# Kernel optimization log

Hardware: AMD Instinct MI355X
Metric: run time of the kernel (lower is better)

## Reference

```python
import jax, jax.numpy as jnp
import numpy as np

G = 1024        # graphs in batch
NPG = 64        # nodes per graph
EPG = 256       # edges per graph
N = G * NPG     # 65536 total nodes
E = G * EPG     # 262144 total edges
IN_CH = 768
CH = 128
RATIO = 0.5
K = int(RATIO * EPG)  # edges reserved as 'causal' per graph


def setup_inputs() -> dict:
    key = jax.random.key(0)
    ks = jax.random.split(key, 10)
    w = lambda k, shape, fan: (jax.random.normal(k, shape, jnp.float32) / np.float32(np.sqrt(fan)))
    x = jax.random.normal(ks[0], (N, IN_CH), jnp.float32)
    # per-graph random edges, offset into the global node index space
    ei = jax.random.randint(ks[1], (2, G, EPG), 0, NPG)
    edge_index = (ei + (jnp.arange(G) * NPG)[None, :, None]).reshape(2, -1).astype(jnp.int32)
    edge_attr = jax.random.uniform(ks[2], (E,), jnp.float32)  # positive edge weights
    batch = jnp.repeat(jnp.arange(G, dtype=jnp.int32), NPG)
    return dict(
        x=x, edge_index=edge_index, edge_attr=edge_attr, batch=batch,
        W1=w(ks[3], (IN_CH, CH), IN_CH), V1=w(ks[4], (IN_CH, CH), IN_CH), b1=jnp.zeros((CH,), jnp.float32),
        W2=w(ks[5], (CH, CH), CH),       V2=w(ks[6], (CH, CH), CH),       b2=jnp.zeros((CH,), jnp.float32),
        mw1=w(ks[7], (2 * CH, 4 * CH), 2 * CH), mb1=jnp.zeros((4 * CH,), jnp.float32),
        mw2=w(ks[8], (4 * CH, 1), 4 * CH),      mb2=jnp.zeros((1,), jnp.float32),
    )


def reference(x, edge_index, edge_attr, batch, W1, V1, b1, W2, V2, b2, mw1, mb1, mw2, mb2):
    row, col = edge_index[0], edge_index[1]
    ew = edge_attr.reshape(-1)

    # gcn_norm (symmetric, no self loops), as used inside ARMAConv
    deg = jnp.zeros((N,), x.dtype).at[col].add(ew)
    dis = jnp.where(deg > 0, jax.lax.rsqrt(jnp.where(deg > 0, deg, 1.0)), 0.0)
    norm = dis[row] * ew * dis[col]  # [E]

    def arma(h, W, V, b):
        # ARMAConv, num_stacks=1, num_layers=1: ReLU(A_hat (h W) + h V + b)
        m = h @ W                                            # [N, C]
        agg = jnp.zeros((N, W.shape[1]), h.dtype).at[col].add(norm[:, None] * m[row])
        return jax.nn.relu(agg + h @ V + b)

    x1 = jax.nn.relu(arma(x, W1, V1, b1))  # outer F.relu (idempotent after internal ReLU)
    x2 = arma(x1, W2, V2, b2)              # [N, CH]

    # edge-gather MLP -> scalar score per edge
    edge_rep = jnp.concatenate([x2[row], x2[col]], axis=-1)          # [E, 2C]
    pred_edge_weight = (jax.nn.relu(edge_rep @ mw1 + mb1) @ mw2 + mb2).reshape(-1)  # [E]

    # per-graph top-k split (batched replacement of the numpy argpartition loop)
    wg = pred_edge_weight.reshape(G, EPG)
    order = jnp.argsort(-wg, axis=1)                                  # descending
    base = (jnp.arange(G) * EPG)[:, None]
    cid = (base + order[:, :K]).reshape(-1)   # causal (reserved) edge ids
    did = (base + order[:, K:]).reshape(-1)   # conf (dropped) edge ids

    causal = (x2, edge_index[:, cid], edge_attr[cid], pred_edge_weight[cid], batch)
    conf = (x2, edge_index[:, did], edge_attr[did], -pred_edge_weight[did], batch)
    return (*causal, *conf, pred_edge_weight)
```

## Files before the change

### kernel.cpp

```cpp
#include <hip/hip_runtime.h>
#include <hip/hip_bf16.h>
#include <stdint.h>

#define G_    1024
#define NPG   64
#define EPG   256
#define N_    (G_*NPG)
#define E_    (G_*EPG)
#define IN_CH 768
#define CH    128
#define KSEL  128
#define HID   512

#define NCH  (N_*CH)
#define GK   (G_*KSEL)
#define OFF0 0
#define OFF1 (OFF0 + NCH)
#define OFF2 (OFF1 + 2*GK)
#define OFF3 (OFF2 + GK)
#define OFF4 (OFF3 + GK)
#define OFF5 (OFF4 + N_)
#define OFF6 (OFF5 + NCH)
#define OFF7 (OFF6 + 2*GK)
#define OFF8 (OFF7 + GK)
#define OFF9 (OFF8 + GK)
#define OFF10 (OFF9 + N_)

typedef unsigned short u16;
typedef unsigned int   u32;
typedef __attribute__((ext_vector_type(8))) short bf16x8;
typedef __attribute__((ext_vector_type(4))) float f32x4;

__device__ __forceinline__ u16 f2bf(float x) {
    union { float f; u32 u; } v; v.f = x;
    u32 r = v.u + 0x7fffu + ((v.u >> 16) & 1u);
    return (u16)(r >> 16);
}
__device__ __forceinline__ float bf2f(u32 h) {
    union { u32 u; float f; } v; v.u = h << 16; return v.f;
}
__device__ __forceinline__ u16 bfc(float x) {
    __hip_bfloat16 h = __float2bfloat16(x);
    return *reinterpret_cast<u16*>(&h);
}

__global__ void k_deg(const int* __restrict__ ei, const float* __restrict__ ea,
                      float* __restrict__ deg) {
    int e = blockIdx.x * 256 + threadIdx.x;
    if (e < E_) atomicAdd(&deg[ei[E_ + e]], ea[e]);
}

__global__ void k_norm(const int* __restrict__ ei, const float* __restrict__ ea,
                       const float* __restrict__ deg, float* __restrict__ norm) {
    int e = blockIdx.x * 256 + threadIdx.x;
    if (e >= E_) return;
    float dr = deg[ei[e]], dc = deg[ei[E_ + e]];
    float fr = dr > 0.f ? 1.0f / sqrtf(dr) : 0.f;
    float fc = dc > 0.f ? 1.0f / sqrtf(dc) : 0.f;
    norm[e] = fr * ea[e] * fc;
}

__global__ void k_concat(const float* __restrict__ W1, const float* __restrict__ V1,
                         const float* __restrict__ W2, const float* __restrict__ V2,
                         const float* __restrict__ mw1,
                         u16* __restrict__ WV1t, u16* __restrict__ WV2t,
                         u16* __restrict__ Mwt) {
    int i = blockIdx.x * 256 + threadIdx.x;
    if (i < 256 * IN_CH) {
        int c = i / IN_CH, r = i - c * IN_CH;
        WV1t[i] = f2bf(c < CH ? W1[r*CH + c] : V1[r*CH + (c - CH)]);
    }
    if (i < 256 * CH) {
        int c = i >> 7, r = i & 127;
        WV2t[i] = f2bf(c < CH ? W2[r*CH + c] : V2[r*CH + (c - CH)]);
    }
    if (i < 1024 * CH) {
        int c = i >> 7, r = i & 127;
        Mwt[i] = f2bf(c < HID ? mw1[r*HID + c] : mw1[(CH + r)*HID + (c - HID)]);
    }
}

__global__ __launch_bounds__(256) void k_gemm1(const float* __restrict__ Ap,
        const u16* __restrict__ Bt, u16* __restrict__ Cp) {
    __shared__ float As[2][128 * 32];
    const int t = threadIdx.x;
    const int lane = t & 63, w = t >> 6;
    const int wr = (w >> 1) << 6, wc = (w & 1) << 6;
    const size_t bm = (size_t)blockIdx.x * 128;
    const size_t bn = (size_t)blockIdx.y * 128;
    const int r16 = lane & 15, kq = lane >> 4;

    int cid[4], grow[4], gcol[4];
    #pragma unroll
    for (int i = 0; i < 4; ++i) {
        int c = i * 256 + t;
        cid[i] = c;
        int row = c >> 3, sl = c & 7;
        grow[i] = row;
        gcol[i] = (sl ^ (row & 7)) * 4;
    }

    f32x4 acc[4][4];
    #pragma unroll
    for (int m = 0; m < 4; ++m)
        #pragma unroll
        for (int n = 0; n < 4; ++n)
            acc[m][n] = (f32x4){0.f, 0.f, 0.f, 0.f};

    #define STAGE(buf, k0)                                                      \
        do {                                                                    \
            _Pragma("unroll")                                                   \
            for (int i = 0; i < 4; ++i) {                                       \
                const float* src = Ap + (bm + grow[i]) * (size_t)IN_CH + (k0) + gcol[i]; \
                __builtin_amdgcn_global_load_lds(                               \
                    (const __attribute__((address_space(1))) void*)src,         \
                    (__attribute__((address_space(3))) void*)&As[buf][cid[i] * 4], \
                    16, 0, 0);                                                  \
            }                                                                   \
        } while (0)

    #define LOADB(bv, k0)                                                       \
        do {                                                                    \
            _Pragma("unroll")                                                   \
            for (int n = 0; n < 4; ++n)                                         \
                bv[n] = *(const bf16x8*)(Bt + (bn + wc + n * 16 + r16) * (size_t)IN_CH + (k0) + kq * 8); \
        } while (0)

    STAGE(0, 0);
    bf16x8 bc[4];
    LOADB(bc, 0);
    __syncthreads();

    const int nk = IN_CH / 32;
    int buf = 0;
    for (int ki = 0; ki < nk; ++ki) {
        bf16x8 bnx[4];
        if (ki + 1 < nk) {
            STAGE(buf ^ 1, (ki + 1) * 32);
            LOADB(bnx, (ki + 1) * 32);
        }
        bf16x8 a[4];
        #pragma unroll
        for (int m = 0; m < 4; ++m) {
            int row = wr + m * 16 + r16;
            int xr = row & 7;
            const float* base = &As[buf][row * 32];
            float4 q0 = *(const float4*)(base + (((2 * kq)     ^ xr) * 4));
            float4 q1 = *(const float4*)(base + (((2 * kq + 1) ^ xr) * 4));
            union { bf16x8 v; u16 s[8]; } pk;
            pk.s[0] = bfc(q0.x); pk.s[1] = bfc(q0.y); pk.s[2] = bfc(q0.z); pk.s[3] = bfc(q0.w);
            pk.s[4] = bfc(q1.x); pk.s[5] = bfc(q1.y); pk.s[6] = bfc(q1.z); pk.s[7] = bfc(q1.w);
            a[m] = pk.v;
        }
        #pragma unroll
        for (int m = 0; m < 4; ++m)
            #pragma unroll
            for (int n = 0; n < 4; ++n)
                acc[m][n] = __builtin_amdgcn_mfma_f32_16x16x32_bf16(a[m], bc[n], acc[m][n], 0, 0, 0);
        if (ki + 1 < nk) {
            #pragma unroll
            for (int n = 0; n < 4; ++n) bc[n] = bnx[n];
        }
        __syncthreads();
        buf ^= 1;
    }
    #undef STAGE
    #undef LOADB

    #pragma unroll
    for (int m = 0; m < 4; ++m)
        #pragma unroll
        for (int j = 0; j < 4; ++j) {
            size_t row = bm + wr + m * 16 + kq * 4 + j;
            #pragma unroll
            for (int n = 0; n < 4; ++n) {
                size_t col = bn + wc + n * 16 + r16;
                Cp[row * 256 + col] = f2bf(acc[m][n][j]);
            }
        }
}

#define PQS 1032
__global__ __launch_bounds__(512) void k_graph(const u16* __restrict__ B1b,
        const u16* __restrict__ WV2t, const u16* __restrict__ Mwt,
        const int* __restrict__ ei, const float* __restrict__ norm,
        const float* __restrict__ b1, const float* __restrict__ b2,
        const float* __restrict__ mb1, const float* __restrict__ mw2,
        const float* __restrict__ mb2, const float* __restrict__ ea,
        float* __restrict__ out) {
    __shared__ char Lds[152576];
    float* A_s   = (float*)(Lds + 0);
    u16*   Ms    = (u16*)(Lds + 16640);
    u16*   x1s   = (u16*)(Lds + 34048);
    u16*   MVs   = (u16*)(Lds + 51456);
    u16*   PQs   = (u16*)(Lds + 0);
    float* mw2s  = (float*)(Lds + 132096);
    u16*   x2s   = (u16*)(Lds + 134144);
    float* predv = (float*)(Lds + 151552);
    float* key   = (float*)(Lds + 0);
    int*   idx   = (int*)(Lds + 1024);

    const int g = blockIdx.x, t = threadIdx.x;
    const int lane = t & 63, w = t >> 6;
    const int r16 = lane & 15, kq = lane >> 4;
    const size_t nbase = (size_t)g * 64;
    union bfr { bf16x8 v; u16 s[8]; };

    if (t < 128) *(float4*)&mw2s[t * 4] = *(const float4*)&mw2[t * 4];
    for (int i = t; i < 64 * 65; i += 512) A_s[i] = 0.f;
    for (int i = t; i < 64 * 32; i += 512) {
        int row = i >> 5, c4 = (i & 31) << 2;
        *(uint2*)&Ms[row * 136 + c4] = *(const uint2*)(B1b + (nbase + row) * 256 + c4);
    }
    int er = 0, ec = 0; float env = 0.f;
    if (t < 256) { int e = g * 256 + t; er = ei[e] & 63; ec = ei[E_ + e] & 63; env = norm[e]; }
    __syncthreads();
    if (t < 256) atomicAdd(&A_s[er * 65 + ec], env);
    __syncthreads();

    {
        const int n0 = w * 16;
        f32x4 acc[4];
        #pragma unroll
        for (int mt = 0; mt < 4; ++mt) acc[mt] = (f32x4){0.f, 0.f, 0.f, 0.f};
        #pragma unroll
        for (int ks = 0; ks < 2; ++ks) {
            bfr a[4], b;
            #pragma unroll
            for (int mt = 0; mt < 4; ++mt)
                #pragma unroll
                for (int i = 0; i < 8; ++i)
                    a[mt].s[i] = f2bf(A_s[(ks*32 + kq*8 + i) * 65 + mt*16 + r16]);
            #pragma unroll
            for (int i = 0; i < 8; ++i)
                b.s[i] = Ms[(ks*32 + kq*8 + i) * 136 + n0 + r16];
            #pragma unroll
            for (int mt = 0; mt < 4; ++mt)
                acc[mt] = __builtin_amdgcn_mfma_f32_16x16x32_bf16(a[mt].v, b.v, acc[mt], 0, 0, 0);
        }
        const int ch = w * 16 + r16;
        #pragma unroll
        for (int mt = 0; mt < 4; ++mt)
            #pragma unroll
            for (int j = 0; j < 4; ++j) {
                int c = mt * 16 + kq * 4 + j;
                float v = bf2f(B1b[(nbase + c) * 256 + 128 + ch]) + b1[ch];
                x1s[c * 136 + ch] = f2bf(fmaxf(acc[mt][j] + v, 0.f));
            }
    }
    __syncthreads();

    {
        const int wc2 = w * 32;
        f32x4 acc[4][2];
        #pragma unroll
        for (int mt = 0; mt < 4; ++mt)
            #pragma unroll
            for (int n = 0; n < 2; ++n) acc[mt][n] = (f32x4){0.f, 0.f, 0.f, 0.f};
        #pragma unroll
        for (int ks = 0; ks < 4; ++ks) {
            bf16x8 a[4], b[2];
            #pragma unroll
            for (int mt = 0; mt < 4; ++mt)
                a[mt] = *(const bf16x8*)&x1s[(mt*16 + r16) * 136 + ks*32 + kq*8];
            #pragma unroll
            for (int n = 0; n < 2; ++n)
                b[n] = *(const bf16x8*)(WV2t + (size_t)(wc2 + n*16 + r16) * 128 + ks*32 + kq*8);
            #pragma unroll
            for (int mt = 0; mt < 4; ++mt)
                #pragma unroll
                for (int n = 0; n < 2; ++n)
                    acc[mt][n] = __builtin_amdgcn_mfma_f32_16x16x32_bf16(a[mt], b[n], acc[mt][n], 0, 0, 0);
        }
        #pragma unroll
        for (int mt = 0; mt < 4; ++mt)
            #pragma unroll
            for (int j = 0; j < 4; ++j) {
                int row = mt * 16 + kq * 4 + j;
                #pragma unroll
                for (int n = 0; n < 2; ++n)
                    MVs[row * 272 + wc2 + n*16 + r16] = f2bf(acc[mt][n][j]);
            }
    }
    __syncthreads();

    {
        const int n0 = w * 16;
        f32x4 acc[4];
        #pragma unroll
        for (int mt = 0; mt < 4; ++mt) acc[mt] = (f32x4){0.f, 0.f, 0.f, 0.f};
        #pragma unroll
        for (int ks = 0; ks < 2; ++ks) {
            bfr a[4], b;
            #pragma unroll
            for (int mt = 0; mt < 4; ++mt)
                #pragma unroll
                for (int i = 0; i < 8; ++i)
                    a[mt].s[i] = f2bf(A_s[(ks*32 + kq*8 + i) * 65 + mt*16 + r16]);
            #pragma unroll
            for (int i = 0; i < 8; ++i)
                b.s[i] = MVs[(ks*32 + kq*8 + i) * 272 + n0 + r16];
            #pragma unroll
            for (int mt = 0; mt < 4; ++mt)
                acc[mt] = __builtin_amdgcn_mfma_f32_16x16x32_bf16(a[mt].v, b.v, acc[mt], 0, 0, 0);
        }
        const int ch = w * 16 + r16;
        #pragma unroll
        for (int mt = 0; mt < 4; ++mt)
            #pragma unroll
            for (int j = 0; j < 4; ++j) {
                int c = mt * 16 + kq * 4 + j;
                float v = bf2f(MVs[c * 272 + 128 + ch]) + b2[ch];
                float r = fmaxf(acc[mt][j] + v, 0.f);
                size_t node = nbase + c;
                out[OFF0 + node * 128 + ch] = r;
                out[OFF5 + node * 128 + ch] = r;
                x2s[c * 136 + ch] = f2bf(r);
            }
    }
    __syncthreads();

    {
        const int nb = w * 128;
        f32x4 acc[4][8];
        #pragma unroll
        for (int mt = 0; mt < 4; ++mt)
            #pragma unroll
            for (int nt = 0; nt < 8; ++nt) acc[mt][nt] = (f32x4){0.f, 0.f, 0.f, 0.f};
        #pragma unroll
        for (int ks = 0; ks < 4; ++ks) {
            bf16x8 a[4], b[8];
            #pragma unroll
            for (int mt = 0; mt < 4; ++mt)
                a[mt] = *(const bf16x8*)&x2s[(mt*16 + r16) * 136 + ks*32 + kq*8];
            #pragma unroll
            for (int nt = 0; nt < 8; ++nt)
                b[nt] = *(const bf16x8*)(Mwt + (size_t)(nb + nt*16 + r16) * 128 + ks*32 + kq*8);
            #pragma unroll
            for (int mt = 0; mt < 4; ++mt)
                #pragma unroll
                for (int nt = 0; nt < 8; ++nt)
                    acc[mt][nt] = __builtin_amdgcn_mfma_f32_16x16x32_bf16(a[mt], b[nt], acc[mt][nt], 0, 0, 0);
        }
        #pragma unroll
        for (int nt = 0; nt < 8; ++nt) {
            int col = nb + nt * 16 + r16;
            float bias = (col < HID) ? mb1[col] : 0.f;
            #pragma unroll
            for (int mt = 0; mt < 4; ++mt)
                #pragma unroll
                for (int j = 0; j < 4; ++j) {
                    int row = mt * 16 + kq * 4 + j;
                    PQs[row * PQS + col] = f2bf(acc[mt][nt][j] + bias);
                }
        }
    }
    __syncthreads();

    {
        const int le = lane & 31, jh = lane >> 5;
        const int eloc = w * 32 + le;
        const int e = g * 256 + eloc;
        const int r = ei[e] & 63, c = ei[E_ + e] & 63;
        const u16* pP = &PQs[r * PQS + jh * 256];
        const u16* pQ = &PQs[c * PQS + 512 + jh * 256];
        const float* pW = &mw2s[jh * 256];
        float s = 0.f;
        #pragma unroll 8
        for (int it = 0; it < 32; ++it) {
            uint4 up = *(const uint4*)(pP + it * 8);
            uint4 uq = *(const uint4*)(pQ + it * 8);
            float4 w0 = *(const float4*)(pW + it * 8);
            float4 w1 = *(const float4*)(pW + it * 8 + 4);
            u32 pu[4] = {up.x, up.y, up.z, up.w};
            u32 qu[4] = {uq.x, uq.y, uq.z, uq.w};
            float ww[8] = {w0.x,w0.y,w0.z,w0.w,w1.x,w1.y,w1.z,w1.w};
            #pragma unroll
            for (int k = 0; k < 4; ++k) {
                float p0 = bf2f(pu[k] & 0xffffu), p1 = bf2f(pu[k] >> 16);
                float q0 = bf2f(qu[k] & 0xffffu), q1 = bf2f(qu[k] >> 16);
                s += fmaxf(p0 + q0, 0.f) * ww[2*k];
                s += fmaxf(p1 + q1, 0.f) * ww[2*k + 1];
            }
        }
        s += __shfl_xor(s, 32, 64);
        if (lane < 32) {
            float pv = s + mb2[0];
            predv[eloc] = pv;
            out[OFF10 + e] = pv;
        }
    }
    __syncthreads();

    if (t < 256) { key[t] = predv[t]; idx[t] = t; }
    for (int k2 = 2; k2 <= 256; k2 <<= 1) {
        for (int j = k2 >> 1; j >= 1; j >>= 1) {
            __syncthreads();
            if (t < 256) {
                int ixj = t ^ j;
                if (ixj > t) {
                    float ka = key[t], kb = key[ixj];
                    int   ia = idx[t], ib = idx[ixj];
                    bool up = ((t & k2) == 0);
                    bool a_before_b = (ka > kb) || (ka == kb && ia < ib);
                    bool do_swap = up ? !a_before_b : a_before_b;
                    if (do_swap) { key[t] = kb; key[ixj] = ka; idx[t] = ib; idx[ixj] = ia; }
                }
            }
        }
    }
    __syncthreads();
    if (t < 256) {
        int el = idx[t];
        int eg = g * 256 + el;
        float pv = key[t];
        float r = (float)ei[eg];
        float c = (float)ei[E_ + eg];
        float av = ea[eg];
        if (t < KSEL) {
            int oo = g * KSEL + t;
            out[OFF1 + oo]      = r;
            out[OFF1 + GK + oo] = c;
            out[OFF2 + oo]      = av;
            out[OFF3 + oo]      = pv;
        } else {
            int oo = g * KSEL + (t - KSEL);
            out[OFF6 + oo]      = r;
            out[OFF6 + GK + oo] = c;
            out[OFF7 + oo]      = av;
            out[OFF8 + oo]      = -pv;
        }
    }
    if (t < 64) {
        out[OFF4 + nbase + t] = (float)g;
        out[OFF9 + nbase + t] = (float)g;
    }
}

extern "C" void kernel_launch(void* const* d_in, const int* in_sizes, int n_in,
                              void* d_out, int out_size, void* d_ws, size_t ws_size,
                              hipStream_t stream) {
    const float* x     = (const float*)d_in[0];
    const int*   ei    = (const int*)  d_in[1];
    const float* ea    = (const float*)d_in[2];
    const float* W1    = (const float*)d_in[4];
    const float* V1    = (const float*)d_in[5];
    const float* b1    = (const float*)d_in[6];
    const float* W2    = (const float*)d_in[7];
    const float* V2    = (const float*)d_in[8];
    const float* b2    = (const float*)d_in[9];
    const float* mw1   = (const float*)d_in[10];
    const float* mb1   = (const float*)d_in[11];
    const float* mw2   = (const float*)d_in[12];
    const float* mb2   = (const float*)d_in[13];
    float* out = (float*)d_out;

    char* ws = (char*)d_ws;
    size_t o = 0;
    float* deg  = (float*)(ws + o); o += (size_t)N_ * 4;
    float* norm = (float*)(ws + o); o += (size_t)E_ * 4;
    u16* WV1t   = (u16*)(ws + o);   o += (size_t)256 * IN_CH * 2;
    u16* WV2t   = (u16*)(ws + o);   o += (size_t)256 * CH * 2;
    u16* Mwt    = (u16*)(ws + o);   o += (size_t)1024 * CH * 2;
    u16* B1b    = (u16*)(ws + o);   o += (size_t)N_ * 256 * 2;

    hipMemsetAsync(deg, 0, (size_t)N_ * 4, stream);
    k_deg <<<E_/256, 256, 0, stream>>>(ei, ea, deg);
    k_norm<<<E_/256, 256, 0, stream>>>(ei, ea, deg, norm);
    k_concat<<<768, 256, 0, stream>>>(W1, V1, W2, V2, mw1, WV1t, WV2t, Mwt);

    dim3 g1(N_/128, 2);
    k_gemm1<<<g1, 256, 0, stream>>>(x, WV1t, B1b);

    k_graph<<<G_, 512, 0, stream>>>(B1b, WV2t, Mwt, ei, norm, b1, b2,
                                    mb1, mw2, mb2, ea, out);
}
```

Measured before the change: 229.4 us.

## Chunk edge-MLP hidden dimension to shrink LDS and raise occupancy

```diff
diff --git a/kernel.cpp b/kernel.cpp
--- a/kernel.cpp
+++ b/kernel.cpp
@@ -180,25 +180,23 @@
         }
 }
 
-#define PQS 1032
-__global__ __launch_bounds__(512) void k_graph(const u16* __restrict__ B1b,
+__global__ __launch_bounds__(512, 4) void k_graph(const u16* __restrict__ B1b,
         const u16* __restrict__ WV2t, const u16* __restrict__ Mwt,
         const int* __restrict__ ei, const float* __restrict__ norm,
         const float* __restrict__ b1, const float* __restrict__ b2,
         const float* __restrict__ mb1, const float* __restrict__ mw2,
         const float* __restrict__ mb2, const float* __restrict__ ea,
         float* __restrict__ out) {
-    __shared__ char Lds[152576];
+    __shared__ char Lds[70912];
     float* A_s   = (float*)(Lds + 0);
-    u16*   Ms    = (u16*)(Lds + 16640);
-    u16*   x1s   = (u16*)(Lds + 34048);
-    u16*   MVs   = (u16*)(Lds + 51456);
-    u16*   PQs   = (u16*)(Lds + 0);
-    float* mw2s  = (float*)(Lds + 132096);
-    u16*   x2s   = (u16*)(Lds + 134144);
-    float* predv = (float*)(Lds + 151552);
     float* key   = (float*)(Lds + 0);
     int*   idx   = (int*)(Lds + 1024);
+    u16*   x1s   = (u16*)(Lds + 16640);
+    u16*   x2s   = (u16*)(Lds + 16640);
+    u16*   Ms    = (u16*)(Lds + 34048);
+    u16*   MVs   = (u16*)(Lds + 34048);
+    u16*   PQc   = (u16*)(Lds + 34048);
+    float* mw2s  = (float*)(Lds + 68864);
 
     const int g = blockIdx.x, t = threadIdx.x;
     const int lane = t & 63, w = t >> 6;
@@ -239,6 +237,7 @@
                 acc[mt] = __builtin_amdgcn_mfma_f32_16x16x32_bf16(a[mt].v, b.v, acc[mt], 0, 0, 0);
         }
         const int ch = w * 16 + r16;
+        __syncthreads();
         #pragma unroll
         for (int mt = 0; mt < 4; ++mt)
             #pragma unroll
@@ -320,79 +319,84 @@
     }
     __syncthreads();
 
-    {
-        const int nb = w * 128;
-        f32x4 acc[4][8];
+    const int le = lane & 31, jh = lane >> 5;
+    const int eloc = w * 32 + le;
+    const int e_g = g * 256 + eloc;
+    const int er6 = ei[e_g] & 63, ec6 = ei[E_ + e_g] & 63;
+    float esum = 0.f;
+    #pragma unroll 1
+    for (int h = 0; h < 4; ++h) {
+        const int wc5 = w * 32;
+        f32x4 acc[4][2];
         #pragma unroll
         for (int mt = 0; mt < 4; ++mt)
             #pragma unroll
-            for (int nt = 0; nt < 8; ++nt) acc[mt][nt] = (f32x4){0.f, 0.f, 0.f, 0.f};
+            for (int n = 0; n < 2; ++n) acc[mt][n] = (f32x4){0.f, 0.f, 0.f, 0.f};
         #pragma unroll
         for (int ks = 0; ks < 4; ++ks) {
-            bf16x8 a[4], b[8];
+            bf16x8 a[4], b[2];
             #pragma unroll
             for (int mt = 0; mt < 4; ++mt)
                 a[mt] = *(const bf16x8*)&x2s[(mt*16 + r16) * 136 + ks*32 + kq*8];
             #pragma unroll
-            for (int nt = 0; nt < 8; ++nt)
-                b[nt] = *(const bf16x8*)(Mwt + (size_t)(nb + nt*16 + r16) * 128 + ks*32 + kq*8);
-            #pragma unroll
-            for (int mt = 0; mt < 4; ++mt)
-                #pragma unroll
-                for (int nt = 0; nt < 8; ++nt)
-                    acc[mt][nt] = __builtin_amdgcn_mfma_f32_16x16x32_bf16(a[mt], b[nt], acc[mt][nt], 0, 0, 0);
-        }
-        #pragma unroll
-        for (int nt = 0; nt < 8; ++nt) {
-            int col = nb + nt * 16 + r16;
-            float bias = (col < HID) ? mb1[col] : 0.f;
+            for (int n = 0; n < 2; ++n) {
+                int colc = wc5 + n * 16 + r16;
+                int mwrow = (colc < 128) ? (h * 128 + colc) : (512 + h * 128 + (colc - 128));
+                b[n] = *(const bf16x8*)(Mwt + (size_t)mwrow * 128 + ks*32 + kq*8);
+            }
+            #pragma unroll
+            for (int mt = 0; mt < 4; ++mt)
+                #pragma unroll
+                for (int n = 0; n < 2; ++n)
+                    acc[mt][n] = __builtin_amdgcn_mfma_f32_16x16x32_bf16(a[mt], b[n], acc[mt][n], 0, 0, 0);
+        }
+        #pragma unroll
+        for (int n = 0; n < 2; ++n) {
+            int colc = wc5 + n * 16 + r16;
+            float bias = (colc < 128) ? mb1[h * 128 + colc] : 0.f;
             #pragma unroll
             for (int mt = 0; mt < 4; ++mt)
                 #pragma unroll
                 for (int j = 0; j < 4; ++j) {
                     int row = mt * 16 + kq * 4 + j;
-                    PQs[row * PQS + col] = f2bf(acc[mt][nt][j] + bias);
+                    PQc[row * 260 + colc] = f2bf(acc[mt][n][j] + bias);
                 }
         }
-    }
-    __syncthreads();
-
+        __syncthreads();
+        {
+            const u16* pP = &PQc[er6 * 260 + jh * 64];
+            const u16* pQ = &PQc[ec6 * 260 + 128 + jh * 64];
+            const float* pW = &mw2s[h * 128 + jh * 64];
+            #pragma unroll
+            for (int it = 0; it < 8; ++it) {
+                uint4 up = *(const uint4*)(pP + it * 8);
+                uint4 uq = *(const uint4*)(pQ + it * 8);
+                float4 w0 = *(const float4*)(pW + it * 8);
+                float4 w1 = *(const float4*)(pW + it * 8 + 4);
+                u32 pu[4] = {up.x, up.y, up.z, up.w};
+                u32 qu[4] = {uq.x, uq.y, uq.z, uq.w};
+                float ww[8] = {w0.x,w0.y,w0.z,w0.w,w1.x,w1.y,w1.z,w1.w};
+                #pragma unroll
+                for (int k = 0; k < 4; ++k) {
+                    float p0 = bf2f(pu[k] & 0xffffu), p1 = bf2f(pu[k] >> 16);
+                    float q0 = bf2f(qu[k] & 0xffffu), q1 = bf2f(qu[k] >> 16);
+                    esum += fmaxf(p0 + q0, 0.f) * ww[2*k];
+                    esum += fmaxf(p1 + q1, 0.f) * ww[2*k + 1];
+                }
+            }
+        }
+        __syncthreads();
+    }
     {
-        const int le = lane & 31, jh = lane >> 5;
-        const int eloc = w * 32 + le;
-        const int e = g * 256 + eloc;
-        const int r = ei[e] & 63, c = ei[E_ + e] & 63;
-        const u16* pP = &PQs[r * PQS + jh * 256];
-        const u16* pQ = &PQs[c * PQS + 512 + jh * 256];
-        const float* pW = &mw2s[jh * 256];
-        float s = 0.f;
-        #pragma unroll 8
-        for (int it = 0; it < 32; ++it) {
-            uint4 up = *(const uint4*)(pP + it * 8);
-            uint4 uq = *(const uint4*)(pQ + it * 8);
-            float4 w0 = *(const float4*)(pW + it * 8);
-            float4 w1 = *(const float4*)(pW + it * 8 + 4);
-            u32 pu[4] = {up.x, up.y, up.z, up.w};
-            u32 qu[4] = {uq.x, uq.y, uq.z, uq.w};
-            float ww[8] = {w0.x,w0.y,w0.z,w0.w,w1.x,w1.y,w1.z,w1.w};
-            #pragma unroll
-            for (int k = 0; k < 4; ++k) {
-                float p0 = bf2f(pu[k] & 0xffffu), p1 = bf2f(pu[k] >> 16);
-                float q0 = bf2f(qu[k] & 0xffffu), q1 = bf2f(qu[k] >> 16);
-                s += fmaxf(p0 + q0, 0.f) * ww[2*k];
-                s += fmaxf(p1 + q1, 0.f) * ww[2*k + 1];
-            }
-        }
-        s += __shfl_xor(s, 32, 64);
+        float s = esum + __shfl_xor(esum, 32, 64);
         if (lane < 32) {
             float pv = s + mb2[0];
-            predv[eloc] = pv;
-            out[OFF10 + e] = pv;
-        }
-    }
-    __syncthreads();
-
-    if (t < 256) { key[t] = predv[t]; idx[t] = t; }
+            out[OFF10 + e_g] = pv;
+            key[eloc] = pv;
+            idx[eloc] = eloc;
+        }
+    }
+
     for (int k2 = 2; k2 <= 256; k2 <<= 1) {
         for (int j = k2 >> 1; j >= 1; j >>= 1) {
             __syncthreads();
```

After: 232.6 us. No clear change (+1.4%).
